# Kernel tuning notes

Hardware: AMD Instinct MI355X
Metric: run time of the kernel (lower is better)

Reference implementation:

```python
import jax, jax.numpy as jnp
import numpy as np

B = 512      # batch per stream
L = 600      # audio length (22 chunks of 75, step 25)
DIM = 256    # model dim
H = 8        # num heads (each head is full-width, per original code)
CH = [1, DIM // 4, DIM // 2, DIM]
KS = [26, 26, 25]
EPS = 1e-5
N_CHUNKS, CHUNK, STEP = 22, 75, 25


def setup_inputs() -> dict:
    key = jax.random.key(0)
    ks = iter(jax.random.split(key, 40))
    def rn(shape, scale=0.05):
        return jax.random.normal(next(ks), shape, jnp.float32) * scale
    inp = {}
    inp["audio_vec1"] = jax.random.normal(next(ks), (B, 1, L), jnp.float32)
    inp["audio_vec2"] = jax.random.normal(next(ks), (B, 1, L), jnp.float32)
    for i in range(3):
        inp[f"conv_w{i+1}"] = rn((CH[i + 1], CH[i], KS[i]))  # OIH, torch Conv1d layout
        inp[f"conv_b{i+1}"] = rn((CH[i + 1],))
        inp[f"bn_g{i+1}"] = jnp.ones((CH[i + 1],), jnp.float32)
        inp[f"bn_b{i+1}"] = jnp.zeros((CH[i + 1],), jnp.float32)
        inp[f"bn_m{i+1}"] = rn((CH[i + 1],))
        inp[f"bn_v{i+1}"] = jnp.ones((CH[i + 1],), jnp.float32)
    # per-head Q/K/V projections (stored [H, in, out]; torch Linear is x @ W.T + b)
    inp["Wq"] = rn((H, DIM, DIM)); inp["bq"] = rn((H, DIM))
    inp["Wk"] = rn((H, DIM, DIM)); inp["bk"] = rn((H, DIM))
    inp["Wv"] = rn((H, DIM, DIM)); inp["bv"] = rn((H, DIM))
    inp["fca_w"] = rn((H * DIM, DIM)); inp["fca_b"] = rn((DIM,))
    inp["fc_w"] = rn((DIM, DIM)); inp["fc_b"] = rn((DIM,))
    return inp


def _chunks(x):
    # x: [B, 1, L] -> [B*22, 1, 75] (batched chunks, chunk-major within each example)
    idx = jnp.arange(N_CHUNKS)[:, None] * STEP + jnp.arange(CHUNK)[None, :]  # [22, 75]
    c = x[:, :, idx]                      # [B, 1, 22, 75]
    return c.transpose(0, 2, 1, 3).reshape(-1, 1, CHUNK)


def _block(x, w, b, g, bt, m, v):
    # Conv1d (valid) + BatchNorm (eval) + Swish; dropout is identity in eval.
    y = jax.lax.conv_general_dilated(
        x, w, window_strides=(1,), padding="VALID",
        dimension_numbers=("NCH", "OIH", "NCH")) + b[None, :, None]
    scale = g * jax.lax.rsqrt(v + EPS)
    y = (y - m[None, :, None]) * scale[None, :, None] + bt[None, :, None]
    return y * jax.nn.sigmoid(y)


def _forward(audio_vec1, audio_vec2,
             conv_w1, conv_b1, bn_g1, bn_b1, bn_m1, bn_v1,
             conv_w2, conv_b2, bn_g2, bn_b2, bn_m2, bn_v2,
             conv_w3, conv_b3, bn_g3, bn_b3, bn_m3, bn_v3,
             Wq, bq, Wk, bk, Wv, bv, fca_w, fca_b, fc_w, fc_b):
    # Batch both streams and all 22 chunks through one conv stack.
    X = jnp.concatenate([_chunks(audio_vec1), _chunks(audio_vec2)], axis=0)  # [2*B*22,1,75]
    X = _block(X, conv_w1, conv_b1, bn_g1, bn_b1, bn_m1, bn_v1)  # [., 64, 50]
    X = _block(X, conv_w2, conv_b2, bn_g2, bn_b2, bn_m2, bn_v2)  # [., 128, 25]
    X = _block(X, conv_w3, conv_b3, bn_g3, bn_b3, bn_m3, bn_v3)  # [., 256, 1]
    feat = X[:, :, 0].reshape(-1, N_CHUNKS, DIM)  # [2B, 22, 256]

    # Multi-head attention: 8 independent full-width heads, no 1/sqrt(d) scaling.
    Q = jnp.einsum("bse,heo->bhso", feat, Wq) + bq[None, :, None, :]
    K = jnp.einsum("bse,heo->bhso", feat, Wk) + bk[None, :, None, :]
    V = jnp.einsum("bse,heo->bhso", feat, Wv) + bv[None, :, None, :]
    A = jax.nn.softmax(jnp.einsum("bhso,bhto->bhst", Q, K), axis=-1)
    O = jnp.einsum("bhst,bhto->bhso", A, V)          # [2B, H, 22, 256]
    O = O.transpose(0, 2, 1, 3).reshape(O.shape[0], N_CHUNKS, H * DIM)
    out = O @ fca_w + fca_b                            # [2B, 22, 256]

    pooled = out.mean(axis=1)                          # [2B, 256]
    y = pooled @ fc_w + fc_b                           # [2B, 256]
    nb = audio_vec1.shape[0]
    return y[:nb], y[nb:]


def reference(audio_vec1, audio_vec2,
              conv_w1, conv_b1, bn_g1, bn_b1, bn_m1, bn_v1,
              conv_w2, conv_b2, bn_g2, bn_b2, bn_m2, bn_v2,
              conv_w3, conv_b3, bn_g3, bn_b3, bn_m3, bn_v3,
              Wq, bq, Wk, bk, Wv, bv, fca_w, fca_b, fc_w, fc_b):
    return _forward(audio_vec1, audio_vec2,
                    conv_w1, conv_b1, bn_g1, bn_b1, bn_m1, bn_v1,
                    conv_w2, conv_b2, bn_g2, bn_b2, bn_m2, bn_v2,
                    conv_w3, conv_b3, bn_g3, bn_b3, bn_m3, bn_v3,
                    Wq, bq, Wk, bk, Wv, bv, fca_w, fca_b, fc_w, fc_b)
```

## Files before the change

kernel.cpp:

```cpp
#include <hip/hip_runtime.h>
#include <hip/hip_bf16.h>
#include <math.h>

#define NSEQ 22528
#define HALFSEQ 11264

typedef __attribute__((ext_vector_type(8))) short short8;
typedef __attribute__((ext_vector_type(4))) float f32x4;
typedef __attribute__((ext_vector_type(4))) ushort ushort4v;

__device__ __forceinline__ ushort f2bf(float x) {
    __hip_bfloat16 h = __float2bfloat16(x);
    return *reinterpret_cast<ushort*>(&h);
}
__device__ __forceinline__ float bf2f(ushort u) {
    unsigned v = ((unsigned)u) << 16;
    return *reinterpret_cast<float*>(&v);
}
__device__ __forceinline__ unsigned pkbf(float lo, float hi) {
    unsigned r;
    asm("v_cvt_pk_bf16_f32 %0, %1, %2" : "=v"(r) : "v"(lo), "v"(hi));
    return r;
}
__device__ __forceinline__ float fsilu(float y) {
    float e = __expf(-y);
    return y * __builtin_amdgcn_rcpf(1.f + e);
}

__global__ __launch_bounds__(256) void k_prep_misc(
    const float* __restrict__ Wk, float* __restrict__ WkT,
    const float* __restrict__ bq, float* __restrict__ kb,
    const float* __restrict__ bv, const float* __restrict__ fca_w,
    const float* __restrict__ fca_b, float* __restrict__ bvc,
    const float* __restrict__ Wv, float* __restrict__ F,
    const float* __restrict__ b3c, const float* __restrict__ g3,
    const float* __restrict__ be3, const float* __restrict__ m3,
    const float* __restrict__ v3, float* __restrict__ sh3)
{
    __shared__ float smem[16 * 256];
    const int bid = blockIdx.x;
    const int tid = threadIdx.x;

    if (bid < 2048) {
        int idx = bid * 256 + tid;
        int b = idx >> 16;
        int rem = idx & 65535;
        int c = rem >> 8;
        int r = rem & 255;
        WkT[idx] = Wk[(size_t)(b * 256 + r) * 256 + c];
    } else if (bid < 2056) {
        int h = bid - 2048;
        smem[tid] = bq[h * 256 + tid];
        __syncthreads();
        const float* wk = Wk + (size_t)(h * 256 + tid) * 256;
        float a = 0.f;
        for (int o = 0; o < 256; ++o) a += wk[o] * smem[o];
        kb[h * 256 + tid] = a;
    } else if (bid < 2057) {
        for (int i = tid; i < 2048; i += 256) smem[i] = bv[i];
        __syncthreads();
        float acc = fca_b[tid];
        for (int k = 0; k < 2048; ++k) acc += smem[k] * fca_w[(size_t)k * 256 + tid];
        bvc[tid] = acc;
    } else if (bid < 2185) {
        int lb = bid - 2057;
        int h = lb >> 4;
        int e0 = (lb & 15) * 16;
        for (int idx = tid; idx < 4096; idx += 256) {
            int r = idx >> 8;
            int c = idx & 255;
            smem[r * 256 + c] = Wv[(size_t)h * 65536 + (e0 + r) * 256 + c];
        }
        __syncthreads();
        float acc[16];
        #pragma unroll
        for (int r = 0; r < 16; ++r) acc[r] = 0.f;
        for (int o = 0; o < 256; ++o) {
            float w = fca_w[(size_t)(h * 256 + o) * 256 + tid];
            #pragma unroll
            for (int r = 0; r < 16; ++r) acc[r] += smem[r * 256 + o] * w;
        }
        #pragma unroll
        for (int r = 0; r < 16; ++r)
            F[(size_t)(h * 256 + e0 + r) * 256 + tid] = acc[r];
    } else {
        float A = g3[tid] * rsqrtf(v3[tid] + 1e-5f);
        sh3[tid] = (b3c[tid] - m3[tid]) * A + be3[tid];
    }
}

__global__ __launch_bounds__(256) void k_prep_w2t(
    const float* __restrict__ w2, ushort* __restrict__ w2f,
    const float* __restrict__ g2, const float* __restrict__ v2)
{
    __shared__ float tile[13312];
    const int mt = blockIdx.x >> 1;
    const int ich = blockIdx.x & 1;
    const int tid = threadIdx.x;
    for (int idx = tid; idx < 13312; idx += 256) {
        int oc16 = idx / 832;
        int rem = idx - oc16 * 832;
        tile[idx] = w2[(size_t)(mt * 16 + oc16) * 1664 + ich * 832 + rem];
    }
    __syncthreads();
    for (int wi = tid; wi < 26 * 512; wi += 256) {
        int t = wi >> 9;
        int li = wi & 511;
        int lane = li >> 3;
        int j = li & 7;
        int oc16 = lane & 15;
        int il = ((lane >> 4) << 3) + j;
        int oc = mt * 16 + oc16;
        float A = g2[oc] * rsqrtf(v2[oc] + 1e-5f);
        w2f[(size_t)(((2 * t + ich) * 8 + mt) << 9) + li] = f2bf(tile[oc16 * 832 + il * 26 + t] * A);
    }
}

__global__ __launch_bounds__(256) void k_prep_w3t(
    const float* __restrict__ w3, ushort* __restrict__ w3f,
    const float* __restrict__ g3, const float* __restrict__ v3)
{
    __shared__ float tile[12800];
    const int mt = blockIdx.x >> 2;
    const int icb = blockIdx.x & 3;
    const int tid = threadIdx.x;
    for (int idx = tid; idx < 12800; idx += 256) {
        int oc16 = idx / 800;
        int rem = idx - oc16 * 800;
        tile[idx] = w3[(size_t)(mt * 16 + oc16) * 3200 + icb * 800 + rem];
    }
    __syncthreads();
    for (int wi = tid; wi < 25 * 512; wi += 256) {
        int pos = wi >> 9;
        int li = wi & 511;
        int lane = li >> 3;
        int j = li & 7;
        int oc16 = lane & 15;
        int il = ((lane >> 4) << 3) + j;
        int oc = mt * 16 + oc16;
        float A = g3[oc] * rsqrtf(v3[oc] + 1e-5f);
        w3f[(size_t)(((pos * 4 + icb) * 16 + mt) << 9) + li] = f2bf(tile[oc16 * 800 + il * 25 + pos] * A);
    }
}

__global__ __launch_bounds__(256) void k_prep_attn_m(
    const float* __restrict__ Wq, const float* __restrict__ WkT,
    float* __restrict__ M)
{
    const int h = blockIdx.x >> 4;
    const int e0 = (blockIdx.x & 15) * 16;
    const int tid = threadIdx.x;
    __shared__ float sq[16][256];
    for (int idx = tid; idx < 4096; idx += 256) {
        int r = idx >> 8;
        int c = idx & 255;
        sq[r][c] = Wq[(size_t)(h * 256 + e0 + r) * 256 + c];
    }
    __syncthreads();
    float acc[16];
    #pragma unroll
    for (int r = 0; r < 16; ++r) acc[r] = 0.f;
    const float* wkt = WkT + (size_t)h * 65536 + tid;
    for (int o = 0; o < 256; ++o) {
        float wk = wkt[o * 256];
        #pragma unroll
        for (int r = 0; r < 16; ++r) acc[r] += sq[r][o] * wk;
    }
    #pragma unroll
    for (int r = 0; r < 16; ++r)
        M[(size_t)(h * 256 + e0 + r) * 256 + tid] = acc[r];
}

__global__ void k_prep_mfrag(const float* __restrict__ M, ushort* __restrict__ Mfrag,
                             const float* __restrict__ kb, ushort* __restrict__ kbf) {
    int bid = blockIdx.x;
    int tid = threadIdx.x;
    if (bid < 2048) {
        int idx = bid * 256 + tid;
        int j = idx & 7;
        int lane = (idx >> 3) & 63;
        int mt = (idx >> 9) & 15;
        int kt = (idx >> 13) & 7;
        int h = idx >> 16;
        int e = kt * 32 + ((lane >> 4) << 3) + j;
        int o = mt * 16 + (lane & 15);
        Mfrag[idx] = f2bf(M[(size_t)(h * 256 + e) * 256 + o]);
    } else {
        int idx = (bid - 2048) * 256 + tid;
        int j = idx & 7;
        int lane = (idx >> 3) & 63;
        int kt = idx >> 9;
        int h = lane & 15;
        int e = kt * 32 + ((lane >> 4) << 3) + j;
        kbf[idx] = (h < 8) ? f2bf(kb[h * 256 + e]) : (ushort)0;
    }
}

__global__ __launch_bounds__(512, 4) void k_conv(
    const float* __restrict__ av1, const float* __restrict__ av2,
    const float* __restrict__ w1,
    const float* __restrict__ b1c, const float* __restrict__ g1,
    const float* __restrict__ be1, const float* __restrict__ m1, const float* __restrict__ v1,
    const ushort* __restrict__ w2f,
    const float* __restrict__ b2c, const float* __restrict__ g2,
    const float* __restrict__ be2, const float* __restrict__ m2, const float* __restrict__ v2,
    ushort* __restrict__ a2f, int seqoff)
{
    __shared__ ushort s_a1[8 * 3208];
    __shared__ ushort s_w1f[2048];
    __shared__ ushort s_xb[8][80];
    __shared__ float s_sh1[64], s_sh2[128];

    const int tid = threadIdx.x;
    const int lane = tid & 63;
    const int w = tid >> 6;
    const int l15 = lane & 15;
    const int grp = lane >> 4;
    const int lseq0 = blockIdx.x * 8;
    const int gseq0 = seqoff + lseq0;

    for (int idx = tid; idx < 640; idx += 512) {
        int s = idx / 80;
        int i = idx - s * 80;
        int seq = gseq0 + s;
        const float* src;
        if (seq < HALFSEQ) { int b = seq / 22; int n = seq - b * 22; src = av1 + b * 600 + n * 25; }
        else { int q = seq - HALFSEQ; int b = q / 22; int n = q - b * 22; src = av2 + b * 600 + n * 25; }
        s_xb[s][i] = f2bf((i < 75) ? src[i] : 0.f);
    }
    for (int idx = tid; idx < 2048; idx += 512) {
        int j = idx & 7;
        int ln = (idx >> 3) & 63;
        int mt = idx >> 9;
        int oc = mt * 16 + (ln & 15);
        int k = ((ln >> 4) << 3) + j;
        float A = g1[oc] * rsqrtf(v1[oc] + 1e-5f);
        s_w1f[idx] = (k < 26) ? f2bf(w1[oc * 26 + k] * A) : (ushort)0;
    }
    if (tid < 64) {
        float A = g1[tid] * rsqrtf(v1[tid] + 1e-5f);
        s_sh1[tid] = (b1c[tid] - m1[tid]) * A + be1[tid];
    }
    if (tid >= 128 && tid < 256) {
        int o = tid - 128;
        float A = g2[o] * rsqrtf(v2[o] + 1e-5f);
        s_sh2[o] = (b2c[o] - m2[o]) * A + be2[o];
    }
    __syncthreads();

    {
        short8 a1f[4];
        #pragma unroll
        for (int mt = 0; mt < 4; ++mt)
            a1f[mt] = *(const short8*)(s_w1f + mt * 512 + lane * 8);

        for (int nt = w; nt < 25; nt += 8) {
            int n = nt * 16 + l15;
            int s = n / 50;
            int p = n - s * 50;
            short8 bf;
            #pragma unroll
            for (int j = 0; j < 8; ++j) {
                int t = grp * 8 + j;
                bf[j] = (t < 26) ? (short)s_xb[s][p + t] : (short)0;
            }
            #pragma unroll
            for (int mt = 0; mt < 4; ++mt) {
                f32x4 acc1 = (f32x4){0.f, 0.f, 0.f, 0.f};
                acc1 = __builtin_amdgcn_mfma_f32_16x16x32_bf16(a1f[mt], bf, acc1, 0, 0, 0);
                int oc0 = mt * 16 + grp * 4;
                int icb = oc0 >> 3;
                int boff = s * 6416 + icb * 800 + p * 16 + (oc0 & 7) * 2;
                float y0 = fsilu(acc1[0] + s_sh1[oc0 + 0]);
                float y1 = fsilu(acc1[1] + s_sh1[oc0 + 1]);
                float y2 = fsilu(acc1[2] + s_sh1[oc0 + 2]);
                float y3 = fsilu(acc1[3] + s_sh1[oc0 + 3]);
                uint2 u;
                u.x = pkbf(y0, y1);
                u.y = pkbf(y2, y3);
                *(uint2*)((char*)s_a1 + boff) = u;
            }
        }
    }
    __syncthreads();

    {
        const int mset = w & 3;
        const int nset = w >> 2;
        const int NT = nset ? 6 : 7;

        int vaddr[7];
        #pragma unroll
        for (int ni = 0; ni < 7; ++ni) {
            int nt = nset * 7 + ni;
            int n = nt * 16 + l15;
            int s = n / 25; if (s > 7) s = 7;
            int p = n - s * 25; if (p > 24) p = 24;
            vaddr[ni] = s * 6416 + grp * 800 + p * 16;
        }

        f32x4 acc[2][7];
        #pragma unroll
        for (int mi = 0; mi < 2; ++mi)
            #pragma unroll
            for (int ni = 0; ni < 7; ++ni)
                acc[mi][ni] = (f32x4){0.f, 0.f, 0.f, 0.f};

        const ushort* wpt = w2f + (size_t)(mset * 2) * 512 + lane * 8;
        short8 afA0 = *(const short8*)(wpt);
        short8 afA1 = *(const short8*)(wpt + 512);
        short8 afB0 = *(const short8*)(wpt + 4096);
        short8 afB1 = *(const short8*)(wpt + 4096 + 512);

        for (int t = 0; t < 26; ++t) {
            #pragma unroll
            for (int ni = 0; ni < 7; ++ni) {
                if (ni >= NT) break;
                short8 bf = *(const short8*)((const char*)s_a1 + vaddr[ni]);
                acc[0][ni] = __builtin_amdgcn_mfma_f32_16x16x32_bf16(afA0, bf, acc[0][ni], 0, 0, 0);
                acc[1][ni] = __builtin_amdgcn_mfma_f32_16x16x32_bf16(afA1, bf, acc[1][ni], 0, 0, 0);
            }
            if (t < 25) {
                afA0 = *(const short8*)(wpt + 8192);
                afA1 = *(const short8*)(wpt + 8192 + 512);
            }
            #pragma unroll
            for (int ni = 0; ni < 7; ++ni) {
                if (ni >= NT) break;
                short8 bf = *(const short8*)((const char*)s_a1 + vaddr[ni] + 3200);
                acc[0][ni] = __builtin_amdgcn_mfma_f32_16x16x32_bf16(afB0, bf, acc[0][ni], 0, 0, 0);
                acc[1][ni] = __builtin_amdgcn_mfma_f32_16x16x32_bf16(afB1, bf, acc[1][ni], 0, 0, 0);
            }
            if (t < 25) {
                afB0 = *(const short8*)(wpt + 12288);
                afB1 = *(const short8*)(wpt + 12288 + 512);
                wpt += 8192;
            }
            #pragma unroll
            for (int ni = 0; ni < 7; ++ni) vaddr[ni] += 16;
        }

        #pragma unroll
        for (int mi = 0; mi < 2; ++mi) {
            const int ocb = mset * 32 + mi * 16 + grp * 4;
            const int grp_dst = (ocb >> 3) & 3;
            const int jb = ocb & 7;
            const int kthi = ocb >> 5;
            #pragma unroll
            for (int ni = 0; ni < 7; ++ni) {
                if (ni >= NT) break;
                int n = (nset * 7 + ni) * 16 + l15;
                if (n < 200) {
                    int s = n / 25;
                    int p = n - s * 25;
                    int seq = lseq0 + s;
                    int kt3 = p * 4 + kthi;
                    float y0 = fsilu(acc[mi][ni][0] + s_sh2[ocb + 0]);
                    float y1 = fsilu(acc[mi][ni][1] + s_sh2[ocb + 1]);
                    float y2 = fsilu(acc[mi][ni][2] + s_sh2[ocb + 2]);
                    float y3 = fsilu(acc[mi][ni][3] + s_sh2[ocb + 3]);
                    uint2 u;
                    u.x = pkbf(y0, y1);
                    u.y = pkbf(y2, y3);
                    *(uint2*)(a2f + (((size_t)(seq >> 4) * 100 + kt3) << 9)
                              + ((seq & 15) + 16 * grp_dst) * 8 + jb) = u;
                }
            }
        }
    }
}

__global__ __launch_bounds__(256) void k_conv3(
    const ushort* __restrict__ a2f, const ushort* __restrict__ w3f,
    const float* __restrict__ sh3,
    float* __restrict__ feat, int seqoff)
{
    const int tid = threadIdx.x;
    const int lane = tid & 63;
    const int wv = tid >> 6;
    const int l15 = lane & 15;
    const int grp = lane >> 4;
    const int lseq0 = blockIdx.x * 64;

    f32x4 acc3[4][4];
    #pragma unroll
    for (int mi = 0; mi < 4; ++mi)
        #pragma unroll
        for (int nt = 0; nt < 4; ++nt)
            acc3[mi][nt] = (f32x4){0.f, 0.f, 0.f, 0.f};

    const ushort* bp = a2f + ((size_t)(lseq0 >> 4) * 100) * 512 + lane * 8;
    const ushort* ap = w3f + (size_t)(wv * 4) * 512 + lane * 8;

    for (int kt = 0; kt < 100; ++kt) {
        short8 bf[4];
        #pragma unroll
        for (int nt = 0; nt < 4; ++nt)
            bf[nt] = *(const short8*)(bp + (size_t)(nt * 100 + kt) * 512);
        #pragma unroll
        for (int mi = 0; mi < 4; ++mi) {
            short8 af = *(const short8*)(ap + (size_t)kt * 8192 + mi * 512);
            #pragma unroll
            for (int nt = 0; nt < 4; ++nt)
                acc3[mi][nt] = __builtin_amdgcn_mfma_f32_16x16x32_bf16(af, bf[nt], acc3[mi][nt], 0, 0, 0);
        }
    }

    #pragma unroll
    for (int nt = 0; nt < 4; ++nt) {
        int gseq = seqoff + lseq0 + nt * 16 + l15;
        #pragma unroll
        for (int mi = 0; mi < 4; ++mi) {
            int oc = wv * 64 + mi * 16 + grp * 4;
            float4 o4;
            #pragma unroll
            for (int r = 0; r < 4; ++r)
                ((float*)&o4)[r] = fsilu(acc3[mi][nt][r] + sh3[oc + r]);
            *(float4*)(feat + (size_t)gseq * 256 + oc) = o4;
        }
    }
}

__global__ __launch_bounds__(512, 2) void k_attn_f(
    const float* __restrict__ feat, const ushort* __restrict__ Mfrag,
    const ushort* __restrict__ kbf, float* __restrict__ fbar_all)
{
    const int g0 = blockIdx.x * 2;
    const int tid = threadIdx.x;
    const int lane = tid & 63;
    const int wv = tid >> 6;
    const int l15 = lane & 15;
    const int grp = lane >> 4;

    __shared__ __align__(16) ushort sfb[2 * 32 * 256];
    __shared__ __align__(16) ushort sG[2 * 32 * 256];
    __shared__ float sS[2 * 528];
    __shared__ float sbet[2 * 192];
    __shared__ float sab[2 * 24];

    char* const sfbb = (char*)sfb;
    char* const sGb = (char*)sG;

    for (int idx = tid; idx < 16384; idx += 512) {
        int gg = idx >> 13;
        int s = (idx >> 8) & 31;
        int e = idx & 255;
        float f = (s < 22) ? feat[(size_t)(g0 + gg) * 5632 + s * 256 + e] : 0.f;
        int byte = gg * 16384 + s * 512 + ((e * 2) ^ ((s & 7) << 4));
        *(ushort*)(sfbb + byte) = f2bf(f);
    }
    __syncthreads();

    if (wv < 4) {
        int gg = wv >> 1;
        int rowb = (wv & 1) * 16;
        int rA = rowb + l15;
        f32x4 acc = (f32x4){0.f, 0.f, 0.f, 0.f};
        for (int kt = 0; kt < 8; ++kt) {
            int e0b = (kt * 32 + grp * 8) * 2;
            short8 af = *(const short8*)(sfbb + gg * 16384 + rA * 512 + (e0b ^ ((rA & 7) << 4)));
            short8 bf = *(const short8*)(kbf + kt * 512 + lane * 8);
            acc = __builtin_amdgcn_mfma_f32_16x16x32_bf16(af, bf, acc, 0, 0, 0);
        }
        #pragma unroll
        for (int r = 0; r < 4; ++r) {
            int t = rowb + grp * 4 + r;
            int h = l15;
            if (t < 22 && h < 8) sbet[gg * 192 + h * 24 + t] = acc[r];
        }
    }
    __syncthreads();

    for (int h = 0; h < 8; ++h) {
        {
            f32x4 accg[4][2];
            #pragma unroll
            for (int mt = 0; mt < 4; ++mt)
                #pragma unroll
                for (int fi = 0; fi < 2; ++fi)
                    accg[mt][fi] = (f32x4){0.f, 0.f, 0.f, 0.f};

            const ushort* mfb = Mfrag + (size_t)h * 65536;
            for (int kt = 0; kt < 8; ++kt) {
                int e0b = (kt * 32 + grp * 8) * 2;
                short8 af[4];
                #pragma unroll
                for (int mt = 0; mt < 4; ++mt) {
                    int gg = mt >> 1;
                    int rA = (mt & 1) * 16 + l15;
                    af[mt] = *(const short8*)(sfbb + gg * 16384 + rA * 512 + (e0b ^ ((rA & 7) << 4)));
                }
                #pragma unroll
                for (int fi = 0; fi < 2; ++fi) {
                    int ft = wv * 2 + fi;
                    short8 bfm = *(const short8*)(mfb + (size_t)((kt * 16 + ft) << 9) + lane * 8);
                    #pragma unroll
                    for (int mt = 0; mt < 4; ++mt)
                        accg[mt][fi] = __builtin_amdgcn_mfma_f32_16x16x32_bf16(af[mt], bfm, accg[mt][fi], 0, 0, 0);
                }
            }
            #pragma unroll
            for (int mt = 0; mt < 4; ++mt) {
                int gg = mt >> 1;
                #pragma unroll
                for (int fi = 0; fi < 2; ++fi) {
                    int f = (wv * 2 + fi) * 16 + l15;
                    #pragma unroll
                    for (int r = 0; r < 4; ++r) {
                        int s = (mt & 1) * 16 + grp * 4 + r;
                        if (s < 22) {
                            int byte = gg * 16384 + s * 512 + ((f * 2) ^ ((s & 7) << 4));
                            *(ushort*)(sGb + byte) = f2bf(accg[mt][fi][r]);
                        }
                    }
                }
            }
        }
        __syncthreads();

        {
            int gg = wv >> 2;
            int mt2 = (wv >> 1) & 1;
            int nt2 = wv & 1;
            f32x4 sacc = (f32x4){0.f, 0.f, 0.f, 0.f};
            int sA = mt2 * 16 + l15;
            int tB = nt2 * 16 + l15;
            for (int kt = 0; kt < 8; ++kt) {
                int f0b = (kt * 32 + grp * 8) * 2;
                short8 ga = *(const short8*)(sGb + gg * 16384 + sA * 512 + (f0b ^ ((sA & 7) << 4)));
                short8 fb = *(const short8*)(sfbb + gg * 16384 + tB * 512 + (f0b ^ ((tB & 7) << 4)));
                sacc = __builtin_amdgcn_mfma_f32_16x16x32_bf16(ga, fb, sacc, 0, 0, 0);
            }
            #pragma unroll
            for (int r = 0; r < 4; ++r) {
                int s = mt2 * 16 + grp * 4 + r;
                int t = nt2 * 16 + l15;
                if (s < 22 && t < 22)
                    sS[gg * 528 + s * 24 + t] = sacc[r] + sbet[gg * 192 + h * 24 + t];
            }
        }
        __syncthreads();

        if (tid < 44) {
            int gg = tid >= 22;
            int s = tid - gg * 22;
            float* row = sS + gg * 528 + s * 24;
            float mx = -1e30f;
            #pragma unroll
            for (int t = 0; t < 22; ++t) mx = fmaxf(mx, row[t]);
            float ex[22];
            float sum = 0.f;
            #pragma unroll
            for (int t = 0; t < 22; ++t) { float e2 = __expf(row[t] - mx); ex[t] = e2; sum += e2; }
            float inv = 1.f / sum;
            #pragma unroll
            for (int t = 0; t < 22; ++t) row[t] = ex[t] * inv;
        }
        __syncthreads();
        if (tid < 44) {
            int gg = tid >= 22;
            int t = tid - gg * 22;
            float a = 0.f;
            #pragma unroll
            for (int s = 0; s < 22; ++s) a += sS[gg * 528 + s * 24 + t];
            sab[gg * 24 + t] = a * (1.f / 22.f);
        }
        __syncthreads();

        {
            int gg = tid >> 8;
            int e = tid & 255;
            int e2b = e * 2;
            float a = 0.f;
            #pragma unroll
            for (int t = 0; t < 22; ++t) {
                ushort u = *(ushort*)(sfbb + gg * 16384 + t * 512 + (e2b ^ ((t & 7) << 4)));
                a += sab[gg * 24 + t] * bf2f(u);
            }
            fbar_all[((size_t)(g0 + gg) * 8 + h) * 256 + e] = a;
        }
        __syncthreads();
    }
}

__global__ __launch_bounds__(256) void k_pool(
    const float* __restrict__ fbar_all, const float* __restrict__ F,
    const float* __restrict__ bvc,
    const float* __restrict__ fc_w, const float* __restrict__ fc_b,
    float* __restrict__ out)
{
    const int g0 = blockIdx.x * 4;
    const int tid = threadIdx.x;
    __shared__ __align__(16) float sfb[4 * 2048];
    __shared__ __align__(16) float sp[4 * 256];
    for (int idx = tid; idx < 8192; idx += 256)
        sfb[idx] = fbar_all[(size_t)g0 * 8 * 256 + idx];
    __syncthreads();

    float p[4];
    float bb = bvc[tid];
    #pragma unroll
    for (int j = 0; j < 4; ++j) p[j] = bb;
    for (int k = 0; k < 2048; k += 4) {
        float f0 = F[(size_t)(k + 0) * 256 + tid];
        float f1 = F[(size_t)(k + 1) * 256 + tid];
        float f2 = F[(size_t)(k + 2) * 256 + tid];
        float f3 = F[(size_t)(k + 3) * 256 + tid];
        #pragma unroll
        for (int j = 0; j < 4; ++j) {
            float4 v = *(const float4*)(sfb + j * 2048 + k);
            p[j] += v.x * f0 + v.y * f1 + v.z * f2 + v.w * f3;
        }
    }
    #pragma unroll
    for (int j = 0; j < 4; ++j) sp[j * 256 + tid] = p[j];
    __syncthreads();

    float y[4];
    float fb = fc_b[tid];
    #pragma unroll
    for (int j = 0; j < 4; ++j) y[j] = fb;
    for (int e = 0; e < 256; ++e) {
        float w = fc_w[(size_t)e * 256 + tid];
        #pragma unroll
        for (int j = 0; j < 4; ++j) y[j] += sp[j * 256 + e] * w;
    }
    #pragma unroll
    for (int j = 0; j < 4; ++j)
        out[(size_t)(g0 + j) * 256 + tid] = y[j];
}

extern "C" void kernel_launch(void* const* d_in, const int* in_sizes, int n_in,
                              void* d_out, int out_size, void* d_ws, size_t ws_size,
                              hipStream_t stream) {
    (void)in_sizes; (void)n_in; (void)out_size;

    const float* av1   = (const float*)d_in[0];
    const float* av2   = (const float*)d_in[1];
    const float* w1    = (const float*)d_in[2];
    const float* b1c   = (const float*)d_in[3];
    const float* g1    = (const float*)d_in[4];
    const float* be1   = (const float*)d_in[5];
    const float* m1    = (const float*)d_in[6];
    const float* v1    = (const float*)d_in[7];
    const float* w2    = (const float*)d_in[8];
    const float* b2c   = (const float*)d_in[9];
    const float* g2    = (const float*)d_in[10];
    const float* be2   = (const float*)d_in[11];
    const float* m2    = (const float*)d_in[12];
    const float* v2    = (const float*)d_in[13];
    const float* w3    = (const float*)d_in[14];
    const float* b3c   = (const float*)d_in[15];
    const float* g3    = (const float*)d_in[16];
    const float* be3   = (const float*)d_in[17];
    const float* m3    = (const float*)d_in[18];
    const float* v3    = (const float*)d_in[19];
    const float* Wq    = (const float*)d_in[20];
    const float* bq    = (const float*)d_in[21];
    const float* Wk    = (const float*)d_in[22];
    const float* bk    = (const float*)d_in[23];
    const float* Wv    = (const float*)d_in[24];
    const float* bv    = (const float*)d_in[25];
    const float* fca_w = (const float*)d_in[26];
    const float* fca_b = (const float*)d_in[27];
    const float* fc_w  = (const float*)d_in[28];
    const float* fc_b  = (const float*)d_in[29];
    (void)bk;

    float* ws = (float*)d_ws;
    float* feat = ws;
    float* Mm   = feat + 5767168;
    float* WkT  = Mm + 524288;
    float* kb   = WkT + 524288;
    float* bvc  = kb + 2048;
    float* F    = bvc + 256;
    float* fbar = F + 524288;
    float* sh3  = fbar + 2097152;
    ushort* w2f = (ushort*)(sh3 + 256);
    ushort* w3f = w2f + 212992;
    ushort* mfr = w3f + 819200;
    ushort* kbf = mfr + 524288;
    ushort* region = kbf + 4096;

    size_t base_bytes = (size_t)((char*)region - (char*)d_ws);
    size_t budget = (ws_size > base_bytes + 4096) ? (ws_size - base_bytes - 4096) : 0;
    int ncA = 16;
    const int cand[5] = {1, 2, 4, 8, 16};
    for (int i = 0; i < 5; ++i) { if ((size_t)144179200 / cand[i] <= budget) { ncA = cand[i]; break; } }
    const int seqsA = NSEQ / ncA;

    k_prep_misc<<<2186, 256, 0, stream>>>(Wk, WkT, bq, kb, bv, fca_w, fca_b, bvc, Wv, F,
                                          b3c, g3, be3, m3, v3, sh3);
    k_prep_w2t<<<16, 256, 0, stream>>>(w2, w2f, g2, v2);
    k_prep_w3t<<<64, 256, 0, stream>>>(w3, w3f, g3, v3);
    k_prep_attn_m<<<128, 256, 0, stream>>>(Wq, WkT, Mm);
    k_prep_mfrag<<<2064, 256, 0, stream>>>(Mm, mfr, kb, kbf);

    ushort* a2f = region;
    for (int c = 0; c < ncA; ++c) {
        int seqoff = c * seqsA;
        k_conv<<<seqsA / 8, 512, 0, stream>>>(av1, av2,
            w1, b1c, g1, be1, m1, v1,
            w2f, b2c, g2, be2, m2, v2,
            a2f, seqoff);
        k_conv3<<<seqsA / 64, 256, 0, stream>>>(a2f, w3f, sh3, feat, seqoff);
    }

    k_attn_f<<<512, 512, 0, stream>>>(feat, mfr, kbf, fbar);
    k_pool<<<256, 256, 0, stream>>>(fbar, F, bvc, fc_w, fc_b, (float*)d_out);
}
```

Before: 553.4 us.

## Merge prep kernels, double-buffer conv3 loads, split attention to one group per block

Three separate changes. The w2/w3/kb packing kernels are merged into one launch, and k_prep_attn_m now writes the bf16 MFMA fragment layout of M directly, which removes the fp32 M buffer and the separate fragment kernel. The conv3 MFMA loop now prefetches the next k-step's A and B fragments into a second register set, to hide global load latency. The attention kernel now uses one group per 256-thread block with a higher occupancy hint instead of two groups per 512-thread block, which changes shared memory per block and the work per wave.

```diff
diff --git a/kernel.cpp b/kernel.cpp
--- a/kernel.cpp
+++ b/kernel.cpp
@@ -89,63 +89,72 @@
     }
 }
 
-__global__ __launch_bounds__(256) void k_prep_w2t(
+__global__ __launch_bounds__(256) void k_prep_packs(
     const float* __restrict__ w2, ushort* __restrict__ w2f,
-    const float* __restrict__ g2, const float* __restrict__ v2)
+    const float* __restrict__ g2, const float* __restrict__ v2,
+    const float* __restrict__ w3, ushort* __restrict__ w3f,
+    const float* __restrict__ g3, const float* __restrict__ v3,
+    const float* __restrict__ kb, ushort* __restrict__ kbf)
 {
     __shared__ float tile[13312];
-    const int mt = blockIdx.x >> 1;
-    const int ich = blockIdx.x & 1;
+    const int bid = blockIdx.x;
     const int tid = threadIdx.x;
-    for (int idx = tid; idx < 13312; idx += 256) {
-        int oc16 = idx / 832;
-        int rem = idx - oc16 * 832;
-        tile[idx] = w2[(size_t)(mt * 16 + oc16) * 1664 + ich * 832 + rem];
-    }
-    __syncthreads();
-    for (int wi = tid; wi < 26 * 512; wi += 256) {
-        int t = wi >> 9;
-        int li = wi & 511;
-        int lane = li >> 3;
-        int j = li & 7;
-        int oc16 = lane & 15;
-        int il = ((lane >> 4) << 3) + j;
-        int oc = mt * 16 + oc16;
-        float A = g2[oc] * rsqrtf(v2[oc] + 1e-5f);
-        w2f[(size_t)(((2 * t + ich) * 8 + mt) << 9) + li] = f2bf(tile[oc16 * 832 + il * 26 + t] * A);
-    }
-}
-
-__global__ __launch_bounds__(256) void k_prep_w3t(
-    const float* __restrict__ w3, ushort* __restrict__ w3f,
-    const float* __restrict__ g3, const float* __restrict__ v3)
-{
-    __shared__ float tile[12800];
-    const int mt = blockIdx.x >> 2;
-    const int icb = blockIdx.x & 3;
-    const int tid = threadIdx.x;
-    for (int idx = tid; idx < 12800; idx += 256) {
-        int oc16 = idx / 800;
-        int rem = idx - oc16 * 800;
-        tile[idx] = w3[(size_t)(mt * 16 + oc16) * 3200 + icb * 800 + rem];
-    }
-    __syncthreads();
-    for (int wi = tid; wi < 25 * 512; wi += 256) {
-        int pos = wi >> 9;
-        int li = wi & 511;
-        int lane = li >> 3;
-        int j = li & 7;
-        int oc16 = lane & 15;
-        int il = ((lane >> 4) << 3) + j;
-        int oc = mt * 16 + oc16;
-        float A = g3[oc] * rsqrtf(v3[oc] + 1e-5f);
-        w3f[(size_t)(((pos * 4 + icb) * 16 + mt) << 9) + li] = f2bf(tile[oc16 * 800 + il * 25 + pos] * A);
+
+    if (bid < 16) {
+        const int mt = bid >> 1;
+        const int ich = bid & 1;
+        for (int idx = tid; idx < 13312; idx += 256) {
+            int oc16 = idx / 832;
+            int rem = idx - oc16 * 832;
+            tile[idx] = w2[(size_t)(mt * 16 + oc16) * 1664 + ich * 832 + rem];
+        }
+        __syncthreads();
+        for (int wi = tid; wi < 26 * 512; wi += 256) {
+            int t = wi >> 9;
+            int li = wi & 511;
+            int lane = li >> 3;
+            int j = li & 7;
+            int oc16 = lane & 15;
+            int il = ((lane >> 4) << 3) + j;
+            int oc = mt * 16 + oc16;
+            float A = g2[oc] * rsqrtf(v2[oc] + 1e-5f);
+            w2f[(size_t)(((2 * t + ich) * 8 + mt) << 9) + li] = f2bf(tile[oc16 * 832 + il * 26 + t] * A);
+        }
+    } else if (bid < 80) {
+        const int lb = bid - 16;
+        const int mt = lb >> 2;
+        const int icb = lb & 3;
+        for (int idx = tid; idx < 12800; idx += 256) {
+            int oc16 = idx / 800;
+            int rem = idx - oc16 * 800;
+            tile[idx] = w3[(size_t)(mt * 16 + oc16) * 3200 + icb * 800 + rem];
+        }
+        __syncthreads();
+        for (int wi = tid; wi < 25 * 512; wi += 256) {
+            int pos = wi >> 9;
+            int li = wi & 511;
+            int lane = li >> 3;
+            int j = li & 7;
+            int oc16 = lane & 15;
+            int il = ((lane >> 4) << 3) + j;
+            int oc = mt * 16 + oc16;
+            float A = g3[oc] * rsqrtf(v3[oc] + 1e-5f);
+            w3f[(size_t)(((pos * 4 + icb) * 16 + mt) << 9) + li] = f2bf(tile[oc16 * 800 + il * 25 + pos] * A);
+        }
+    } else {
+        int idx = (bid - 80) * 256 + tid;
+        int j = idx & 7;
+        int lane = (idx >> 3) & 63;
+        int kt = idx >> 9;
+        int h = lane & 15;
+        int e = kt * 32 + ((lane >> 4) << 3) + j;
+        kbf[idx] = (h < 8) ? f2bf(kb[h * 256 + e]) : (ushort)0;
     }
 }
 
 __global__ __launch_bounds__(256) void k_prep_attn_m(
     const float* __restrict__ Wq, const float* __restrict__ WkT,
-    float* __restrict__ M)
+    ushort* __restrict__ Mfrag)
 {
     const int h = blockIdx.x >> 4;
     const int e0 = (blockIdx.x & 15) * 16;
@@ -166,33 +175,16 @@
         #pragma unroll
         for (int r = 0; r < 16; ++r) acc[r] += sq[r][o] * wk;
     }
-    #pragma unroll
-    for (int r = 0; r < 16; ++r)
-        M[(size_t)(h * 256 + e0 + r) * 256 + tid] = acc[r];
-}
-
-__global__ void k_prep_mfrag(const float* __restrict__ M, ushort* __restrict__ Mfrag,
-                             const float* __restrict__ kb, ushort* __restrict__ kbf) {
-    int bid = blockIdx.x;
-    int tid = threadIdx.x;
-    if (bid < 2048) {
-        int idx = bid * 256 + tid;
-        int j = idx & 7;
-        int lane = (idx >> 3) & 63;
-        int mt = (idx >> 9) & 15;
-        int kt = (idx >> 13) & 7;
-        int h = idx >> 16;
-        int e = kt * 32 + ((lane >> 4) << 3) + j;
-        int o = mt * 16 + (lane & 15);
-        Mfrag[idx] = f2bf(M[(size_t)(h * 256 + e) * 256 + o]);
-    } else {
-        int idx = (bid - 2048) * 256 + tid;
-        int j = idx & 7;
-        int lane = (idx >> 3) & 63;
-        int kt = idx >> 9;
-        int h = lane & 15;
-        int e = kt * 32 + ((lane >> 4) << 3) + j;
-        kbf[idx] = (h < 8) ? f2bf(kb[h * 256 + e]) : (ushort)0;
+    const int o = tid;
+    const int mt = o >> 4;
+    const int ob = o & 15;
+    #pragma unroll
+    for (int r = 0; r < 16; ++r) {
+        int e = e0 + r;
+        int kt = e >> 5;
+        int lane = ob + 16 * ((e >> 3) & 3);
+        int j = e & 7;
+        Mfrag[(size_t)h * 65536 + (size_t)(kt * 16 + mt) * 512 + lane * 8 + j] = f2bf(acc[r]);
     }
 }
 
@@ -392,18 +384,33 @@
     const ushort* bp = a2f + ((size_t)(lseq0 >> 4) * 100) * 512 + lane * 8;
     const ushort* ap = w3f + (size_t)(wv * 4) * 512 + lane * 8;
 
-    for (int kt = 0; kt < 100; ++kt) {
-        short8 bf[4];
-        #pragma unroll
-        for (int nt = 0; nt < 4; ++nt)
-            bf[nt] = *(const short8*)(bp + (size_t)(nt * 100 + kt) * 512);
-        #pragma unroll
-        for (int mi = 0; mi < 4; ++mi) {
-            short8 af = *(const short8*)(ap + (size_t)kt * 8192 + mi * 512);
+    short8 bfA[4], bfB[4], afA[4], afB[4];
+    #pragma unroll
+    for (int nt = 0; nt < 4; ++nt) bfA[nt] = *(const short8*)(bp + (size_t)(nt * 100) * 512);
+    #pragma unroll
+    for (int mi = 0; mi < 4; ++mi) afA[mi] = *(const short8*)(ap + mi * 512);
+
+    for (int kt = 0; kt < 100; kt += 2) {
+        #pragma unroll
+        for (int nt = 0; nt < 4; ++nt) bfB[nt] = *(const short8*)(bp + (size_t)(nt * 100 + kt + 1) * 512);
+        #pragma unroll
+        for (int mi = 0; mi < 4; ++mi) afB[mi] = *(const short8*)(ap + (size_t)(kt + 1) * 8192 + mi * 512);
+        #pragma unroll
+        for (int mi = 0; mi < 4; ++mi)
             #pragma unroll
             for (int nt = 0; nt < 4; ++nt)
-                acc3[mi][nt] = __builtin_amdgcn_mfma_f32_16x16x32_bf16(af, bf[nt], acc3[mi][nt], 0, 0, 0);
-        }
+                acc3[mi][nt] = __builtin_amdgcn_mfma_f32_16x16x32_bf16(afA[mi], bfA[nt], acc3[mi][nt], 0, 0, 0);
+        if (kt < 98) {
+            #pragma unroll
+            for (int nt = 0; nt < 4; ++nt) bfA[nt] = *(const short8*)(bp + (size_t)(nt * 100 + kt + 2) * 512);
+            #pragma unroll
+            for (int mi = 0; mi < 4; ++mi) afA[mi] = *(const short8*)(ap + (size_t)(kt + 2) * 8192 + mi * 512);
+        }
+        #pragma unroll
+        for (int mi = 0; mi < 4; ++mi)
+            #pragma unroll
+            for (int nt = 0; nt < 4; ++nt)
+                acc3[mi][nt] = __builtin_amdgcn_mfma_f32_16x16x32_bf16(afB[mi], bfB[nt], acc3[mi][nt], 0, 0, 0);
     }
 
     #pragma unroll
@@ -421,95 +428,86 @@
     }
 }
 
-__global__ __launch_bounds__(512, 2) void k_attn_f(
+__global__ __launch_bounds__(256, 4) void k_attn_f(
     const float* __restrict__ feat, const ushort* __restrict__ Mfrag,
     const ushort* __restrict__ kbf, float* __restrict__ fbar_all)
 {
-    const int g0 = blockIdx.x * 2;
+    const int g = blockIdx.x;
     const int tid = threadIdx.x;
     const int lane = tid & 63;
     const int wv = tid >> 6;
     const int l15 = lane & 15;
     const int grp = lane >> 4;
 
-    __shared__ __align__(16) ushort sfb[2 * 32 * 256];
-    __shared__ __align__(16) ushort sG[2 * 32 * 256];
-    __shared__ float sS[2 * 528];
-    __shared__ float sbet[2 * 192];
-    __shared__ float sab[2 * 24];
+    __shared__ __align__(16) ushort sfb[32 * 256];
+    __shared__ __align__(16) ushort sG[32 * 256];
+    __shared__ float sS[528];
+    __shared__ float sbet[192];
+    __shared__ float sab[24];
 
     char* const sfbb = (char*)sfb;
     char* const sGb = (char*)sG;
 
-    for (int idx = tid; idx < 16384; idx += 512) {
-        int gg = idx >> 13;
-        int s = (idx >> 8) & 31;
+    for (int idx = tid; idx < 8192; idx += 256) {
+        int s = idx >> 8;
         int e = idx & 255;
-        float f = (s < 22) ? feat[(size_t)(g0 + gg) * 5632 + s * 256 + e] : 0.f;
-        int byte = gg * 16384 + s * 512 + ((e * 2) ^ ((s & 7) << 4));
+        float f = (s < 22) ? feat[(size_t)g * 5632 + s * 256 + e] : 0.f;
+        int byte = s * 512 + ((e * 2) ^ ((s & 7) << 4));
         *(ushort*)(sfbb + byte) = f2bf(f);
     }
     __syncthreads();
 
-    if (wv < 4) {
-        int gg = wv >> 1;
-        int rowb = (wv & 1) * 16;
-        int rA = rowb + l15;
+    if (wv < 2) {
+        int rA = wv * 16 + l15;
         f32x4 acc = (f32x4){0.f, 0.f, 0.f, 0.f};
         for (int kt = 0; kt < 8; ++kt) {
             int e0b = (kt * 32 + grp * 8) * 2;
-            short8 af = *(const short8*)(sfbb + gg * 16384 + rA * 512 + (e0b ^ ((rA & 7) << 4)));
+            short8 af = *(const short8*)(sfbb + rA * 512 + (e0b ^ ((rA & 7) << 4)));
             short8 bf = *(const short8*)(kbf + kt * 512 + lane * 8);
             acc = __builtin_amdgcn_mfma_f32_16x16x32_bf16(af, bf, acc, 0, 0, 0);
         }
         #pragma unroll
         for (int r = 0; r < 4; ++r) {
-            int t = rowb + grp * 4 + r;
+            int t = wv * 16 + grp * 4 + r;
             int h = l15;
-            if (t < 22 && h < 8) sbet[gg * 192 + h * 24 + t] = acc[r];
+            if (t < 22 && h < 8) sbet[h * 24 + t] = acc[r];
         }
     }
     __syncthreads();
 
     for (int h = 0; h < 8; ++h) {
         {
-            f32x4 accg[4][2];
-            #pragma unroll
-            for (int mt = 0; mt < 4; ++mt)
+            f32x4 accg[2][4];
+            #pragma unroll
+            for (int mt = 0; mt < 2; ++mt)
                 #pragma unroll
-                for (int fi = 0; fi < 2; ++fi)
+                for (int fi = 0; fi < 4; ++fi)
                     accg[mt][fi] = (f32x4){0.f, 0.f, 0.f, 0.f};
 
             const ushort* mfb = Mfrag + (size_t)h * 65536;
             for (int kt = 0; kt < 8; ++kt) {
                 int e0b = (kt * 32 + grp * 8) * 2;
-                short8 af[4];
+                int rA0 = l15, rA1 = 16 + l15;
+                short8 af0 = *(const short8*)(sfbb + rA0 * 512 + (e0b ^ ((rA0 & 7) << 4)));
+                short8 af1 = *(const short8*)(sfbb + rA1 * 512 + (e0b ^ ((rA1 & 7) << 4)));
                 #pragma unroll
-                for (int mt = 0; mt < 4; ++mt) {
-                    int gg = mt >> 1;
-                    int rA = (mt & 1) * 16 + l15;
-                    af[mt] = *(const short8*)(sfbb + gg * 16384 + rA * 512 + (e0b ^ ((rA & 7) << 4)));
+                for (int fi = 0; fi < 4; ++fi) {
+                    int ft = wv * 4 + fi;
+                    short8 bfm = *(const short8*)(mfb + (size_t)((kt * 16 + ft) << 9) + lane * 8);
+                    accg[0][fi] = __builtin_amdgcn_mfma_f32_16x16x32_bf16(af0, bfm, accg[0][fi], 0, 0, 0);
+                    accg[1][fi] = __builtin_amdgcn_mfma_f32_16x16x32_bf16(af1, bfm, accg[1][fi], 0, 0, 0);
                 }
+            }
+            #pragma unroll
+            for (int mt = 0; mt < 2; ++mt) {
                 #pragma unroll
-                for (int fi = 0; fi < 2; ++fi) {
-                    int ft = wv * 2 + fi;
-                    short8 bfm = *(const short8*)(mfb + (size_t)((kt * 16 + ft) << 9) + lane * 8);
-                    #pragma unroll
-                    for (int mt = 0; mt < 4; ++mt)
-                        accg[mt][fi] = __builtin_amdgcn_mfma_f32_16x16x32_bf16(af[mt], bfm, accg[mt][fi], 0, 0, 0);
-                }
-            }
-            #pragma unroll
-            for (int mt = 0; mt < 4; ++mt) {
-                int gg = mt >> 1;
-                #pragma unroll
-                for (int fi = 0; fi < 2; ++fi) {
-                    int f = (wv * 2 + fi) * 16 + l15;
+                for (int fi = 0; fi < 4; ++fi) {
+                    int f = (wv * 4 + fi) * 16 + l15;
                     #pragma unroll
                     for (int r = 0; r < 4; ++r) {
-                        int s = (mt & 1) * 16 + grp * 4 + r;
+                        int s = mt * 16 + grp * 4 + r;
                         if (s < 22) {
-                            int byte = gg * 16384 + s * 512 + ((f * 2) ^ ((s & 7) << 4));
+                            int byte = s * 512 + ((f * 2) ^ ((s & 7) << 4));
                             *(ushort*)(sGb + byte) = f2bf(accg[mt][fi][r]);
                         }
                     }
@@ -519,16 +517,15 @@
         __syncthreads();
 
         {
-            int gg = wv >> 2;
-            int mt2 = (wv >> 1) & 1;
+            int mt2 = wv >> 1;
             int nt2 = wv & 1;
             f32x4 sacc = (f32x4){0.f, 0.f, 0.f, 0.f};
             int sA = mt2 * 16 + l15;
             int tB = nt2 * 16 + l15;
             for (int kt = 0; kt < 8; ++kt) {
                 int f0b = (kt * 32 + grp * 8) * 2;
-                short8 ga = *(const short8*)(sGb + gg * 16384 + sA * 512 + (f0b ^ ((sA & 7) << 4)));
-                short8 fb = *(const short8*)(sfbb + gg * 16384 + tB * 512 + (f0b ^ ((tB & 7) << 4)));
+                short8 ga = *(const short8*)(sGb + sA * 512 + (f0b ^ ((sA & 7) << 4)));
+                short8 fb = *(const short8*)(sfbb + tB * 512 + (f0b ^ ((tB & 7) << 4)));
                 sacc = __builtin_amdgcn_mfma_f32_16x16x32_bf16(ga, fb, sacc, 0, 0, 0);
             }
             #pragma unroll
@@ -536,15 +533,13 @@
                 int s = mt2 * 16 + grp * 4 + r;
                 int t = nt2 * 16 + l15;
                 if (s < 22 && t < 22)
-                    sS[gg * 528 + s * 24 + t] = sacc[r] + sbet[gg * 192 + h * 24 + t];
-            }
-        }
-        __syncthreads();
-
-        if (tid < 44) {
-            int gg = tid >= 22;
-            int s = tid - gg * 22;
-            float* row = sS + gg * 528 + s * 24;
+                    sS[s * 24 + t] = sacc[r] + sbet[h * 24 + t];
+            }
+        }
+        __syncthreads();
+
+        if (tid < 22) {
+            float* row = sS + tid * 24;
             float mx = -1e30f;
             #pragma unroll
             for (int t = 0; t < 22; ++t) mx = fmaxf(mx, row[t]);
@@ -557,27 +552,24 @@
             for (int t = 0; t < 22; ++t) row[t] = ex[t] * inv;
         }
         __syncthreads();
-        if (tid < 44) {
-            int gg = tid >= 22;
-            int t = tid - gg * 22;
+        if (tid < 22) {
+            int t = tid;
             float a = 0.f;
             #pragma unroll
-            for (int s = 0; s < 22; ++s) a += sS[gg * 528 + s * 24 + t];
-            sab[gg * 24 + t] = a * (1.f / 22.f);
+            for (int s = 0; s < 22; ++s) a += sS[s * 24 + t];
+            sab[t] = a * (1.f / 22.f);
         }
         __syncthreads();
 
         {
-            int gg = tid >> 8;
-            int e = tid & 255;
-            int e2b = e * 2;
+            int e2b = tid * 2;
             float a = 0.f;
             #pragma unroll
             for (int t = 0; t < 22; ++t) {
-                ushort u = *(ushort*)(sfbb + gg * 16384 + t * 512 + (e2b ^ ((t & 7) << 4)));
-                a += sab[gg * 24 + t] * bf2f(u);
-            }
-            fbar_all[((size_t)(g0 + gg) * 8 + h) * 256 + e] = a;
+                ushort u = *(ushort*)(sfbb + t * 512 + (e2b ^ ((t & 7) << 4)));
+                a += sab[t] * bf2f(u);
+            }
+            fbar_all[((size_t)g * 8 + h) * 256 + tid] = a;
         }
         __syncthreads();
     }
@@ -669,8 +661,7 @@
 
     float* ws = (float*)d_ws;
     float* feat = ws;
-    float* Mm   = feat + 5767168;
-    float* WkT  = Mm + 524288;
+    float* WkT  = feat + 5767168;
     float* kb   = WkT + 524288;
     float* bvc  = kb + 2048;
     float* F    = bvc + 256;
@@ -691,10 +682,8 @@
 
     k_prep_misc<<<2186, 256, 0, stream>>>(Wk, WkT, bq, kb, bv, fca_w, fca_b, bvc, Wv, F,
                                           b3c, g3, be3, m3, v3, sh3);
-    k_prep_w2t<<<16, 256, 0, stream>>>(w2, w2f, g2, v2);
-    k_prep_w3t<<<64, 256, 0, stream>>>(w3, w3f, g3, v3);
-    k_prep_attn_m<<<128, 256, 0, stream>>>(Wq, WkT, Mm);
-    k_prep_mfrag<<<2064, 256, 0, stream>>>(Mm, mfr, kb, kbf);
+    k_prep_packs<<<96, 256, 0, stream>>>(w2, w2f, g2, v2, w3, w3f, g3, v3, kb, kbf);
+    k_prep_attn_m<<<128, 256, 0, stream>>>(Wq, WkT, mfr);
 
     ushort* a2f = region;
     for (int c = 0; c < ncA; ++c) {
@@ -706,6 +695,6 @@
         k_conv3<<<seqsA / 64, 256, 0, stream>>>(a2f, w3f, sh3, feat, seqoff);
     }
 
-    k_attn_f<<<512, 512, 0, stream>>>(feat, mfr, kbf, fbar);
+    k_attn_f<<<1024, 256, 0, stream>>>(feat, mfr, kbf, fbar);
     k_pool<<<256, 256, 0, stream>>>(fbar, F, bvc, fc_w, fc_b, (float*)d_out);
 }
```

Result: slower. 580.8 us (+4.9%).
